# Kernel tuning notes

Measured on AMD Instinct MI355X. Metric: run time of the kernel, lower is better.

Reference implementation:

```python
import jax, jax.numpy as jnp
import numpy as np

B, IN_DIM, MEM = 8192, 4096, 256
MIN_TS, MAX_TS, EPS = 0.1, 10.0, 1e-6
LN_EPS = 1e-5


def setup_inputs() -> dict:
    key = jax.random.key(0)
    ks = jax.random.split(key, 10)
    std = 0.02
    d_in = MEM + IN_DIM  # 4352
    return {
        "x": jax.random.normal(ks[0], (B, IN_DIM), jnp.float32),
        "h": jax.random.normal(ks[1], (B, MEM), jnp.float32),
        # memory_target: Linear(d_in, 2*MEM) -> LN -> GELU -> Linear(2*MEM, MEM)
        "W1": std * jax.random.normal(ks[2], (d_in, 2 * MEM), jnp.float32),
        "b1": jnp.zeros((2 * MEM,), jnp.float32),
        "g1": jnp.ones((2 * MEM,), jnp.float32),
        "be1": jnp.zeros((2 * MEM,), jnp.float32),
        "W2": std * jax.random.normal(ks[3], (2 * MEM, MEM), jnp.float32),
        "b2": jnp.zeros((MEM,), jnp.float32),
        # decay_gate: Linear(d_in, MEM) -> sigmoid
        "Wd": std * jax.random.normal(ks[4], (d_in, MEM), jnp.float32),
        "bd": jnp.zeros((MEM,), jnp.float32),
        # input_gate: Linear(d_in, MEM) -> sigmoid
        "Wu": std * jax.random.normal(ks[5], (d_in, MEM), jnp.float32),
        "bu": jnp.zeros((MEM,), jnp.float32),
    }


def _layernorm(t, g, b):
    mu = jnp.mean(t, axis=-1, keepdims=True)
    var = jnp.mean(jnp.square(t - mu), axis=-1, keepdims=True)
    return (t - mu) * jax.lax.rsqrt(var + LN_EPS) * g + b


def reference(x, h, W1, b1, g1, be1, W2, b2, Wd, bd, Wu, bu):
    combined = jnp.concatenate([h, x], axis=-1)  # [B, MEM+IN_DIM]
    # memory_target branch: Linear -> LayerNorm -> GELU (exact) -> Linear -> tanh
    t = _layernorm(combined @ W1 + b1, g1, be1)
    t = jax.nn.gelu(t, approximate=False)
    h_candidate = jnp.tanh(t @ W2 + b2)  # [B, MEM]
    # gates
    decay = jax.nn.sigmoid(combined @ Wd + bd)
    update = jax.nn.sigmoid(combined @ Wu + bu)
    decay = MIN_TS + (MAX_TS - MIN_TS) * decay + EPS
    new_h = (1.0 - update) * (h / decay) + update * h_candidate
    # normalize_memory: rescale new_h to old h's L2 norm
    h_norm = jnp.maximum(jnp.linalg.norm(h, axis=-1, keepdims=True), EPS)
    nh_norm = jnp.maximum(jnp.linalg.norm(new_h, axis=-1, keepdims=True), 1e-12)
    new_h = new_h / nh_norm * h_norm
    return new_h
```

## Files before the change

kernel.cpp:

```cpp
#include <hip/hip_runtime.h>
#include <stdint.h>

typedef unsigned short u16;

#define B_ROWS 8192
#define IN_DIM 4096
#define MEM 256
#define D_IN 4352
#define N1 1024
#define K2 512
#define LN_EPS 1e-5f

typedef __attribute__((ext_vector_type(4))) float f32x4;
typedef __attribute__((ext_vector_type(4))) uint32_t u32x4;
typedef __attribute__((ext_vector_type(4))) unsigned short u16x4;
typedef __attribute__((ext_vector_type(8))) short bf16x8;

#define AS1(p) ((__attribute__((address_space(1))) void*)(p))
#define AS3(p) ((__attribute__((address_space(3))) void*)(p))

__device__ __forceinline__ float bf2f(u16 u) {
  union { uint32_t u; float f; } c; c.u = ((uint32_t)u) << 16; return c.f;
}
__device__ __forceinline__ u16 f2bf(float f) {
  union { float f; uint32_t u; } c; c.f = f;
  uint32_t r = (c.u + 0x7fffu + ((c.u >> 16) & 1u)) >> 16;
  return (u16)r;
}
__device__ __forceinline__ uint32_t fbits(float f) {
  union { float f; uint32_t u; } c; c.f = f; return c.u;
}
__device__ __forceinline__ uint32_t pack_rne(float a, float b) {
  return ((uint32_t)f2bf(b) << 16) | f2bf(a);
}
__device__ __forceinline__ uint32_t pack_trunc(float a, float b) {
  return (fbits(b) & 0xFFFF0000u) | (fbits(a) >> 16);
}

__global__ __launch_bounds__(256)
void prep_kernel(const float* __restrict__ W1, const float* __restrict__ Wd,
                 const float* __restrict__ Wu, const float* __restrict__ W2,
                 const float* __restrict__ h, const float* __restrict__ x,
                 u16* __restrict__ WT, u16* __restrict__ W2F, u16* __restrict__ Abf,
                 int pre) {
  __shared__ u16 tile[64][68];
  const int blk = blockIdx.x, t = threadIdx.x;
  if (blk < 1088) {
    int n0 = (blk & 15) * 64, k0 = (blk >> 4) * 64;
    const float* src; int srcN, ns0;
    if (n0 < 512)      { src = W1; srcN = 512; ns0 = n0; }
    else if (n0 < 768) { src = Wd; srcN = 256; ns0 = n0 - 512; }
    else               { src = Wu; srcN = 256; ns0 = n0 - 768; }
    int rr = t >> 4;
    int c4 = (t & 15) * 4;
#pragma unroll
    for (int i = 0; i < 4; i++) {
      int k = i * 16 + rr;
      f32x4 v = *(const f32x4*)&src[(size_t)(k0 + k) * srcN + ns0 + c4];
      tile[c4 + 0][k] = f2bf(v[0]);
      tile[c4 + 1][k] = f2bf(v[1]);
      tile[c4 + 2][k] = f2bf(v[2]);
      tile[c4 + 3][k] = f2bf(v[3]);
    }
    __syncthreads();
#pragma unroll
    for (int i = 0; i < 4; i++) {
      int n = i * 16 + rr;
      u16x4 w;
      w.x = tile[n][c4 + 0];
      w.y = tile[n][c4 + 1];
      w.z = tile[n][c4 + 2];
      w.w = tile[n][c4 + 3];
      if (pre) {
        int n16 = (n0 >> 4) + i;
        int kg = k0 + c4;
        int kstep = kg >> 5;
        int qq = (kg >> 3) & 3;
        int j0 = kg & 7;
        *(u16x4*)&WT[((size_t)(kstep * 64 + n16) * 64 + qq * 16 + rr) * 8 + j0] = w;
      } else {
        *(u16x4*)&WT[(size_t)(n0 + n) * D_IN + k0 + c4] = w;
      }
    }
  } else if (blk < 1104) {
    int kw = blk - 1088;
#pragma unroll
    for (int q = 0; q < 4; q++) {
      float v[8];
#pragma unroll
      for (int j = 0; j < 8; j++)
        v[j] = W2[(size_t)(kw * 32 + q * 8 + j) * 256 + t];
      u32x4 w;
      w.x = pack_rne(v[0], v[1]);
      w.y = pack_rne(v[2], v[3]);
      w.z = pack_rne(v[4], v[5]);
      w.w = pack_rne(v[6], v[7]);
      *(u32x4*)&W2F[(size_t)((kw * 4 + q) * 256 + t) * 8] = w;
    }
  } else {
    int b = blk - 1104;
    const float* src; int r, dcol;
    if (b < 1024) {
      int g = (b * 256 + t) * 8;
      src = h + g; r = g >> 8; dcol = g & 255;
    } else {
      int g = ((b - 1024) * 256 + t) * 8;
      src = x + g; r = g >> 12; dcol = MEM + (g & 4095);
    }
    f32x4 v0 = *(const f32x4*)src;
    f32x4 v1 = *(const f32x4*)(src + 4);
    u32x4 w;
    w.x = pack_rne(v0[0], v0[1]);
    w.y = pack_rne(v0[2], v0[3]);
    w.z = pack_rne(v1[0], v1[1]);
    w.w = pack_rne(v1[2], v1[3]);
    *(u32x4*)&Abf[(size_t)r * D_IN + dcol] = w;
  }
}

#define BAR() { asm volatile("" ::: "memory"); __builtin_amdgcn_s_barrier(); asm volatile("" ::: "memory"); }
#define VMW4() asm volatile("s_waitcnt vmcnt(4)" ::: "memory");

__global__ __launch_bounds__(512, 2)
void gemm1_pre256_kernel(const u16* __restrict__ Abf, const u16* __restrict__ WTF,
                         u16* __restrict__ G0, u16* __restrict__ G1, int klen) {
  __shared__ __attribute__((aligned(16))) u16 As[2][16384];
  const int t = threadIdx.x;
  const int lane = t & 63, wave = t >> 6;
  const int bid = (int)blockIdx.x;
  const int xcd = bid & 7;
  const int idx = bid >> 3;
  const int part = xcd >> 2;
  const int by = (xcd & 3) * 8 + (idx & 7);
  const int bx = idx >> 3;
  const int kbase = part * klen;
  u16* __restrict__ Gout = part ? G1 : G0;
  const int row0 = by * 256, col0 = bx * 256;
  const int q = lane >> 4, mrow = lane & 15;
  const int wm = wave >> 2, wn = wave & 3;
  const int NT = klen >> 6;

  int sr0, sc0_, sr1, sc1_;
  {
    int idx0 = t;        sr0 = idx0 >> 2; sc0_ = (idx0 & 3) ^ ((sr0 >> 1) & 3);
    int idx1 = 512 + t;  sr1 = idx1 >> 2; sc1_ = (idx1 & 3) ^ ((sr1 >> 1) & 3);
  }
  const u16* pa0 = Abf + (size_t)(row0 + sr0) * D_IN + sc0_ * 8;
  const u16* pa1 = Abf + (size_t)(row0 + sr1) * D_IN + sc1_ * 8;
  const int fsw = (mrow >> 1) & 3;

#define STAGE_A(buf, kk, kt)                                                            \
  __builtin_amdgcn_global_load_lds(AS1(pa0 + (kt) + (kk) * 32),                         \
      AS3(&As[buf][(kk) * 8192 + t * 8]), 16, 0, 0);                                    \
  __builtin_amdgcn_global_load_lds(AS1(pa1 + (kt) + (kk) * 32),                         \
      AS3(&As[buf][(kk) * 8192 + (512 + t) * 8]), 16, 0, 0);

  const u16* bptr = WTF + (size_t)(kbase >> 5) * 32768 + (bx * 16 + wn * 4) * 512 + lane * 8;

  f32x4 acc[8][4] = {};
  bf16x8 b0[4], b1[4];

  STAGE_A(0, 0, kbase)
  STAGE_A(0, 1, kbase)
#pragma unroll
  for (int nt = 0; nt < 4; nt++) b0[nt] = *(const bf16x8*)(bptr + nt * 512);
  VMW4();
  BAR();

  for (int tt = 0; tt < NT; ++tt) {
    const int cur = tt & 1, nxt = cur ^ 1;
    const int kn = kbase + (tt + 1) * 64;
    const bool pf = (tt + 1 < NT);

#pragma unroll
    for (int nt = 0; nt < 4; nt++) b1[nt] = *(const bf16x8*)(bptr + 32768 + nt * 512);
    if (pf) { STAGE_A(nxt, 0, kn) }

#define READ_A(kk, mh, areg)                                                            \
  _Pragma("unroll") for (int i = 0; i < 4; i++) {                                       \
    int arow = wm * 128 + ((mh) * 4 + i) * 16 + mrow;                                   \
    areg[i] = *(const bf16x8*)&As[cur][(kk) * 8192 + arow * 32 + (q ^ fsw) * 8];        \
  }
#define MFMA16(mh, breg)                                                                \
  __builtin_amdgcn_s_setprio(1);                                                        \
  _Pragma("unroll") for (int i = 0; i < 4; i++)                                         \
    _Pragma("unroll") for (int nt = 0; nt < 4; nt++)                                    \
      acc[(mh) * 4 + i][nt] =                                                           \
          __builtin_amdgcn_mfma_f32_16x16x32_bf16(a[i], breg[nt], acc[(mh) * 4 + i][nt], 0, 0, 0); \
  __builtin_amdgcn_s_setprio(0);

    {
      bf16x8 a[4];
      READ_A(0, 0, a)
      MFMA16(0, b0)
      READ_A(0, 1, a)
      MFMA16(1, b0)
    }
    if (pf) {
      STAGE_A(nxt, 1, kn)
#pragma unroll
      for (int nt = 0; nt < 4; nt++) b0[nt] = *(const bf16x8*)(bptr + 65536 + nt * 512);
    }
    {
      bf16x8 a[4];
      READ_A(1, 0, a)
      MFMA16(0, b1)
      READ_A(1, 1, a)
      MFMA16(1, b1)
    }
    if (pf) {
      VMW4();
      BAR();
    }
    bptr += 65536;
#undef READ_A
#undef MFMA16
  }

#pragma unroll
  for (int mt = 0; mt < 8; mt++) {
#pragma unroll
    for (int nt = 0; nt < 4; nt++) {
#pragma unroll
      for (int i = 0; i < 4; i++) {
        int row = row0 + wm * 128 + mt * 16 + q * 4 + i;
        int col = col0 + wn * 64 + nt * 16 + mrow;
        Gout[(size_t)row * N1 + col] = f2bf(acc[mt][nt][i]);
      }
    }
  }
}
#undef STAGE_A

__global__ __launch_bounds__(256, 4)
void gemm1_inline_kernel(const float* __restrict__ x, const float* __restrict__ h,
                         const u16* __restrict__ WT, u16* __restrict__ G0,
                         u16* __restrict__ G1, int klen) {
  __shared__ __attribute__((aligned(16))) u16 As[128 * 64];
  __shared__ __attribute__((aligned(16))) u16 Bs[128 * 64];
  const int t = threadIdx.x;
  const int lane = t & 63, wave = t >> 6;
  const int by = blockIdx.x & 63;
  const int bx = (blockIdx.x >> 6) & 7;
  const int part = blockIdx.x >> 9;
  const int kbase = part * klen;
  u16* __restrict__ Gout = part ? G1 : G0;
  const int row0 = by * 128, col0 = bx * 128;
  const int q = lane >> 4, mrow = lane & 15;
  const int wm = wave >> 1, wn = wave & 1;

  int ar[4], ac[4];
#pragma unroll
  for (int j = 0; j < 4; j++) {
    int idx = j * 256 + t;
    int r = idx >> 3;
    ar[j] = r;
    ac[j] = (idx & 7) ^ (r & 7);
  }
  f32x4 acc[4][4] = {};
  for (int k0 = kbase; k0 < kbase + klen; k0 += 64) {
#pragma unroll
    for (int j = 0; j < 4; j++) {
      const u16* gp = WT + (size_t)(col0 + ar[j]) * D_IN + k0 + ac[j] * 8;
      __builtin_amdgcn_global_load_lds(AS1(gp), AS3(&Bs[(j * 256 + t) * 8]), 16, 0, 0);
    }
#pragma unroll
    for (int j = 0; j < 4; j++) {
      int k = k0 + ac[j] * 8;
      const float* gp = (k < MEM) ? (h + (size_t)(row0 + ar[j]) * MEM + k)
                                  : (x + (size_t)(row0 + ar[j]) * IN_DIM + (k - MEM));
      f32x4 v0 = *(const f32x4*)gp;
      f32x4 v1 = *(const f32x4*)(gp + 4);
      u32x4 w;
      w.x = pack_trunc(v0[0], v0[1]);
      w.y = pack_trunc(v0[2], v0[3]);
      w.z = pack_trunc(v1[0], v1[1]);
      w.w = pack_trunc(v1[2], v1[3]);
      *(u32x4*)&As[(j * 256 + t) * 8] = w;
    }
    __syncthreads();
#pragma unroll
    for (int kk = 0; kk < 2; kk++) {
      bf16x8 a[4], b[4];
#pragma unroll
      for (int mt = 0; mt < 4; mt++) {
        int row = wm * 64 + mt * 16 + mrow;
        int p = (kk * 4 + q) ^ (mrow & 7);
        a[mt] = *(const bf16x8*)&As[row * 64 + p * 8];
      }
#pragma unroll
      for (int nt = 0; nt < 4; nt++) {
        int row = wn * 64 + nt * 16 + mrow;
        int p = (kk * 4 + q) ^ (mrow & 7);
        b[nt] = *(const bf16x8*)&Bs[row * 64 + p * 8];
      }
#pragma unroll
      for (int mt = 0; mt < 4; mt++) {
#pragma unroll
        for (int nt = 0; nt < 4; nt++) {
          acc[mt][nt] = __builtin_amdgcn_mfma_f32_16x16x32_bf16(a[mt], b[nt], acc[mt][nt], 0, 0, 0);
        }
      }
    }
    __syncthreads();
  }
#pragma unroll
  for (int mt = 0; mt < 4; mt++) {
#pragma unroll
    for (int nt = 0; nt < 4; nt++) {
#pragma unroll
      for (int i = 0; i < 4; i++) {
        int row = row0 + wm * 64 + mt * 16 + q * 4 + i;
        int col = col0 + wn * 64 + nt * 16 + mrow;
        Gout[(size_t)row * N1 + col] = f2bf(acc[mt][nt][i]);
      }
    }
  }
}

__global__ __launch_bounds__(256, 4)
void fused_ln_gemm2_kernel(const u16* __restrict__ G0, const u16* __restrict__ G1,
                           const u16* __restrict__ W2F, const float* __restrict__ h,
                           const float* __restrict__ b1v, const float* __restrict__ g1v,
                           const float* __restrict__ be1v, const float* __restrict__ b2,
                           const float* __restrict__ bd, const float* __restrict__ bu,
                           float* __restrict__ out, int nparts) {
  __shared__ __attribute__((aligned(16))) u16 As[16 * 512];
  __shared__ float redA[16][4], redB[16][4], scl[16];
  const int t = threadIdx.x, lane = t & 63, wave = t >> 6;
  const int q = lane >> 4, mrow = lane & 15;
  const int r0 = blockIdx.x * 16;

  {
    const int lr = t & 15;
    const int lc = t >> 4;
    float z[32];
    const u16* g0p = G0 + (size_t)(r0 + lr) * N1 + lc * 32;
    const u16* g1p = G1 + (size_t)(r0 + lr) * N1 + lc * 32;
    float s = 0.f, ss = 0.f;
#pragma unroll
    for (int j = 0; j < 4; j++) {
      u32x4 w0 = *(const u32x4*)(g0p + j * 8);
      u32x4 w1;
      if (nparts == 2) w1 = *(const u32x4*)(g1p + j * 8);
#pragma unroll
      for (int e = 0; e < 4; e++) {
        float lo = bf2f((u16)(w0[e] & 0xffff));
        float hi = bf2f((u16)(w0[e] >> 16));
        if (nparts == 2) {
          lo += bf2f((u16)(w1[e] & 0xffff));
          hi += bf2f((u16)(w1[e] >> 16));
        }
        int cb = lc * 32 + j * 8 + e * 2;
        lo += b1v[cb];
        hi += b1v[cb + 1];
        z[j * 8 + e * 2] = lo;
        z[j * 8 + e * 2 + 1] = hi;
        s += lo + hi;
        ss += lo * lo + hi * hi;
      }
    }
    s += __shfl_xor(s, 16, 64);  s += __shfl_xor(s, 32, 64);
    ss += __shfl_xor(ss, 16, 64); ss += __shfl_xor(ss, 32, 64);
    if (lane < 16) { redA[lr][wave] = s; redB[lr][wave] = ss; }
    __syncthreads();
    float S  = redA[lr][0] + redA[lr][1] + redA[lr][2] + redA[lr][3];
    float SS = redB[lr][0] + redB[lr][1] + redB[lr][2] + redB[lr][3];
    float mu = S * (1.0f / 512.0f);
    float var = SS * (1.0f / 512.0f) - mu * mu;
    float rstd = rsqrtf(var + LN_EPS);
#pragma unroll
    for (int j = 0; j < 4; j++) {
      u32x4 wpk;
#pragma unroll
      for (int e = 0; e < 4; e++) {
        int cb = lc * 32 + j * 8 + e * 2;
        float y0 = (z[j * 8 + e * 2] - mu) * rstd * g1v[cb] + be1v[cb];
        float y1 = (z[j * 8 + e * 2 + 1] - mu) * rstd * g1v[cb + 1] + be1v[cb + 1];
        float o0 = 0.5f * y0 * (1.0f + erff(y0 * 0.7071067811865475f));
        float o1 = 0.5f * y1 * (1.0f + erff(y1 * 0.7071067811865475f));
        wpk[e] = pack_rne(o0, o1);
      }
      int p = lc * 4 + j;
      int ps = p ^ (lr & 7);
      *(u32x4*)&As[lr * 512 + ps * 8] = wpk;
    }
  }
  __syncthreads();

  f32x4 acc[4] = {};
#pragma unroll
  for (int kw = 0; kw < 16; kw++) {
    int pa = (kw * 4 + q) ^ (mrow & 7);
    bf16x8 a = *(const bf16x8*)&As[mrow * 512 + pa * 8];
#pragma unroll
    for (int nt = 0; nt < 4; nt++) {
      const u16* bp = W2F + (size_t)((kw * 4 + q) * 256 + wave * 64 + nt * 16 + mrow) * 8;
      bf16x8 b = *(const bf16x8*)bp;
      acc[nt] = __builtin_amdgcn_mfma_f32_16x16x32_bf16(a, b, acc[nt], 0, 0, 0);
    }
  }
  __syncthreads();

  float snh[4], shh[4];
#pragma unroll
  for (int i = 0; i < 4; i++) {
    int r = q * 4 + i;
    size_t grow = (size_t)(r0 + r);
    float a_nh = 0.f, a_h = 0.f;
#pragma unroll
    for (int nt = 0; nt < 4; nt++) {
      int c = wave * 64 + nt * 16 + mrow;
      float hc = tanhf(acc[nt][i] + b2[c]);
      float zd = bf2f(G0[grow * N1 + 512 + c]);
      float zu = bf2f(G0[grow * N1 + 768 + c]);
      if (nparts == 2) {
        zd += bf2f(G1[grow * N1 + 512 + c]);
        zu += bf2f(G1[grow * N1 + 768 + c]);
      }
      zd += bd[c];
      zu += bu[c];
      float dec = 0.1f + 9.9f / (1.0f + expf(-zd)) + 1e-6f;
      float u = 1.0f / (1.0f + expf(-zu));
      float hv = h[grow * MEM + c];
      float nh = (1.0f - u) * (hv / dec) + u * hc;
      acc[nt][i] = nh;
      a_nh += nh * nh;
      a_h += hv * hv;
    }
    snh[i] = a_nh;
    shh[i] = a_h;
  }
#pragma unroll
  for (int m = 1; m <= 8; m <<= 1) {
#pragma unroll
    for (int i = 0; i < 4; i++) {
      snh[i] += __shfl_xor(snh[i], m, 64);
      shh[i] += __shfl_xor(shh[i], m, 64);
    }
  }
  if (mrow == 0) {
#pragma unroll
    for (int i = 0; i < 4; i++) {
      int r = q * 4 + i;
      redA[r][wave] = snh[i];
      redB[r][wave] = shh[i];
    }
  }
  __syncthreads();
  if (t < 16) {
    float tn = redA[t][0] + redA[t][1] + redA[t][2] + redA[t][3];
    float th = redB[t][0] + redB[t][1] + redB[t][2] + redB[t][3];
    float hn = fmaxf(sqrtf(th), 1e-6f);
    float nn = fmaxf(sqrtf(tn), 1e-12f);
    scl[t] = hn / nn;
  }
  __syncthreads();
#pragma unroll
  for (int i = 0; i < 4; i++) {
    int r = q * 4 + i;
    size_t grow = (size_t)(r0 + r);
    float sc = scl[r];
#pragma unroll
    for (int nt = 0; nt < 4; nt++) {
      int c = wave * 64 + nt * 16 + mrow;
      out[grow * MEM + c] = acc[nt][i] * sc;
    }
  }
}

extern "C" void kernel_launch(void* const* d_in, const int* in_sizes, int n_in,
                              void* d_out, int out_size, void* d_ws, size_t ws_size,
                              hipStream_t stream) {
  const float* x   = (const float*)d_in[0];
  const float* h   = (const float*)d_in[1];
  const float* W1  = (const float*)d_in[2];
  const float* b1  = (const float*)d_in[3];
  const float* g1  = (const float*)d_in[4];
  const float* be1 = (const float*)d_in[5];
  const float* W2  = (const float*)d_in[6];
  const float* b2  = (const float*)d_in[7];
  const float* Wd  = (const float*)d_in[8];
  const float* bd  = (const float*)d_in[9];
  const float* Wu  = (const float*)d_in[10];
  const float* bu  = (const float*)d_in[11];
  float* out = (float*)d_out;

  char* ws = (char*)d_ws;
  u16* WT  = (u16*)(ws);
  u16* W2F = (u16*)(ws + 8912896);
  u16* G0  = (u16*)(ws + 9175040);
  u16* G1  = (u16*)(ws + 25952256);
  u16* Abf = (u16*)(ws + 42729472);

  const int nparts = (ws_size >= 42729472u) ? 2 : 1;
  const int klen = D_IN / nparts;
  const bool use_pre = (ws_size >= 114032640u) && (nparts == 2);

  if (use_pre) {
    prep_kernel<<<18512, 256, 0, stream>>>(W1, Wd, Wu, W2, h, x, WT, W2F, Abf, 1);
    gemm1_pre256_kernel<<<256, 512, 0, stream>>>(Abf, WT, G0, G1, klen);
  } else {
    prep_kernel<<<1104, 256, 0, stream>>>(W1, Wd, Wu, W2, h, x, WT, W2F, Abf, 0);
    gemm1_inline_kernel<<<512 * nparts, 256, 0, stream>>>(x, h, WT, G0, G1, klen);
  }

  fused_ln_gemm2_kernel<<<B_ROWS / 16, 256, 0, stream>>>(G0, G1, W2F, h, b1, g1, be1,
                                                         b2, bd, bu, out, nparts);
}
```

Before: 346.5 us.

## Pre-tile bf16 activations into MFMA fragment layout and load A directly to registers

The prep kernel now writes the bf16 activation matrix in a K-chunked layout of 32-wide fragments, so each lane's MFMA A-operand is one contiguous 16-byte load. The GEMM1 kernel drops the LDS staging of A (global_load_lds, swizzle, barriers) and double-buffers both A and B fragments directly in registers across 32-wide K steps. This removes LDS traffic and synchronisation but raises register pressure, since 16 A fragments plus 8 B fragments are live per thread. Each wave also reloads A rows from global/L2 with no sharing through LDS, which may add global memory traffic.

```diff
diff --git a/kernel.cpp b/kernel.cpp
--- a/kernel.cpp
+++ b/kernel.cpp
@@ -99,13 +99,13 @@
     }
   } else {
     int b = blk - 1104;
-    const float* src; int r, dcol;
+    const float* src; int r, k0;
     if (b < 1024) {
       int g = (b * 256 + t) * 8;
-      src = h + g; r = g >> 8; dcol = g & 255;
+      src = h + g; r = g >> 8; k0 = g & 255;
     } else {
       int g = ((b - 1024) * 256 + t) * 8;
-      src = x + g; r = g >> 12; dcol = MEM + (g & 4095);
+      src = x + g; r = g >> 12; k0 = MEM + (g & 4095);
     }
     f32x4 v0 = *(const f32x4*)src;
     f32x4 v1 = *(const f32x4*)(src + 4);
@@ -114,17 +114,14 @@
     w.y = pack_rne(v0[2], v0[3]);
     w.z = pack_rne(v1[0], v1[1]);
     w.w = pack_rne(v1[2], v1[3]);
-    *(u32x4*)&Abf[(size_t)r * D_IN + dcol] = w;
-  }
-}
-
-#define BAR() { asm volatile("" ::: "memory"); __builtin_amdgcn_s_barrier(); asm volatile("" ::: "memory"); }
-#define VMW4() asm volatile("s_waitcnt vmcnt(4)" ::: "memory");
+    size_t off = ((size_t)(k0 >> 5) * 8192 + r) * 32 + (size_t)((k0 >> 3) & 3) * 8;
+    *(u32x4*)&Abf[off] = w;
+  }
+}
 
 __global__ __launch_bounds__(512, 2)
-void gemm1_pre256_kernel(const u16* __restrict__ Abf, const u16* __restrict__ WTF,
-                         u16* __restrict__ G0, u16* __restrict__ G1, int klen) {
-  __shared__ __attribute__((aligned(16))) u16 As[2][16384];
+void gemm1_reg_kernel(const u16* __restrict__ AF, const u16* __restrict__ WTF,
+                      u16* __restrict__ G0, u16* __restrict__ G1, int klen) {
   const int t = threadIdx.x;
   const int lane = t & 63, wave = t >> 6;
   const int bid = (int)blockIdx.x;
@@ -133,89 +130,56 @@
   const int part = xcd >> 2;
   const int by = (xcd & 3) * 8 + (idx & 7);
   const int bx = idx >> 3;
-  const int kbase = part * klen;
   u16* __restrict__ Gout = part ? G1 : G0;
   const int row0 = by * 256, col0 = bx * 256;
   const int q = lane >> 4, mrow = lane & 15;
   const int wm = wave >> 2, wn = wave & 3;
-  const int NT = klen >> 6;
-
-  int sr0, sc0_, sr1, sc1_;
-  {
-    int idx0 = t;        sr0 = idx0 >> 2; sc0_ = (idx0 & 3) ^ ((sr0 >> 1) & 3);
-    int idx1 = 512 + t;  sr1 = idx1 >> 2; sc1_ = (idx1 & 3) ^ ((sr1 >> 1) & 3);
-  }
-  const u16* pa0 = Abf + (size_t)(row0 + sr0) * D_IN + sc0_ * 8;
-  const u16* pa1 = Abf + (size_t)(row0 + sr1) * D_IN + sc1_ * 8;
-  const int fsw = (mrow >> 1) & 3;
-
-#define STAGE_A(buf, kk, kt)                                                            \
-  __builtin_amdgcn_global_load_lds(AS1(pa0 + (kt) + (kk) * 32),                         \
-      AS3(&As[buf][(kk) * 8192 + t * 8]), 16, 0, 0);                                    \
-  __builtin_amdgcn_global_load_lds(AS1(pa1 + (kt) + (kk) * 32),                         \
-      AS3(&As[buf][(kk) * 8192 + (512 + t) * 8]), 16, 0, 0);
-
-  const u16* bptr = WTF + (size_t)(kbase >> 5) * 32768 + (bx * 16 + wn * 4) * 512 + lane * 8;
+  const int NH = klen >> 5;
+  const int ks0 = part * NH;
+
+  const u16* abase = AF + ((size_t)(row0 + wm * 128 + mrow) * 4 + q) * 8 +
+                     (size_t)ks0 * 262144;
+  const u16* bbase = WTF + (size_t)(bx * 16 + wn * 4) * 512 + lane * 8 +
+                     (size_t)ks0 * 32768;
 
   f32x4 acc[8][4] = {};
-  bf16x8 b0[4], b1[4];
-
-  STAGE_A(0, 0, kbase)
-  STAGE_A(0, 1, kbase)
-#pragma unroll
-  for (int nt = 0; nt < 4; nt++) b0[nt] = *(const bf16x8*)(bptr + nt * 512);
-  VMW4();
-  BAR();
-
-  for (int tt = 0; tt < NT; ++tt) {
-    const int cur = tt & 1, nxt = cur ^ 1;
-    const int kn = kbase + (tt + 1) * 64;
-    const bool pf = (tt + 1 < NT);
-
-#pragma unroll
-    for (int nt = 0; nt < 4; nt++) b1[nt] = *(const bf16x8*)(bptr + 32768 + nt * 512);
-    if (pf) { STAGE_A(nxt, 0, kn) }
-
-#define READ_A(kk, mh, areg)                                                            \
-  _Pragma("unroll") for (int i = 0; i < 4; i++) {                                       \
-    int arow = wm * 128 + ((mh) * 4 + i) * 16 + mrow;                                   \
-    areg[i] = *(const bf16x8*)&As[cur][(kk) * 8192 + arow * 32 + (q ^ fsw) * 8];        \
-  }
-#define MFMA16(mh, breg)                                                                \
-  __builtin_amdgcn_s_setprio(1);                                                        \
-  _Pragma("unroll") for (int i = 0; i < 4; i++)                                         \
-    _Pragma("unroll") for (int nt = 0; nt < 4; nt++)                                    \
-      acc[(mh) * 4 + i][nt] =                                                           \
-          __builtin_amdgcn_mfma_f32_16x16x32_bf16(a[i], breg[nt], acc[(mh) * 4 + i][nt], 0, 0, 0); \
+  bf16x8 aA[8], aB[8], bA[4], bB[4];
+
+#define LOADA(bank, hh) {                                                     \
+    size_t ko = (size_t)(hh) * 262144;                                        \
+    _Pragma("unroll") for (int mt = 0; mt < 8; mt++)                          \
+      bank[mt] = *(const bf16x8*)(abase + ko + mt * 512);                     \
+  }
+#define LOADB(bank, hh) {                                                     \
+    size_t ko = (size_t)(hh) * 32768;                                         \
+    _Pragma("unroll") for (int nt = 0; nt < 4; nt++)                          \
+      bank[nt] = *(const bf16x8*)(bbase + ko + nt * 512);                     \
+  }
+#define MFMA32(abank, bbank)                                                  \
+  __builtin_amdgcn_s_setprio(1);                                              \
+  _Pragma("unroll") for (int mt = 0; mt < 8; mt++)                            \
+    _Pragma("unroll") for (int nt = 0; nt < 4; nt++)                          \
+      acc[mt][nt] = __builtin_amdgcn_mfma_f32_16x16x32_bf16(                  \
+          abank[mt], bbank[nt], acc[mt][nt], 0, 0, 0);                        \
   __builtin_amdgcn_s_setprio(0);
 
-    {
-      bf16x8 a[4];
-      READ_A(0, 0, a)
-      MFMA16(0, b0)
-      READ_A(0, 1, a)
-      MFMA16(1, b0)
-    }
-    if (pf) {
-      STAGE_A(nxt, 1, kn)
-#pragma unroll
-      for (int nt = 0; nt < 4; nt++) b0[nt] = *(const bf16x8*)(bptr + 65536 + nt * 512);
-    }
-    {
-      bf16x8 a[4];
-      READ_A(1, 0, a)
-      MFMA16(0, b1)
-      READ_A(1, 1, a)
-      MFMA16(1, b1)
-    }
-    if (pf) {
-      VMW4();
-      BAR();
-    }
-    bptr += 65536;
-#undef READ_A
-#undef MFMA16
-  }
+  LOADA(aA, 0)
+  LOADB(bA, 0)
+
+  for (int hh = 0; hh < NH; hh += 2) {
+    int h1 = (hh + 1 < NH) ? hh + 1 : hh;
+    LOADA(aB, h1)
+    LOADB(bB, h1)
+    MFMA32(aA, bA)
+    int h2 = (hh + 2 < NH) ? hh + 2 : hh;
+    LOADA(aA, h2)
+    LOADB(bA, h2)
+    MFMA32(aB, bB)
+    __builtin_amdgcn_s_barrier();
+  }
+#undef LOADA
+#undef LOADB
+#undef MFMA32
 
 #pragma unroll
   for (int mt = 0; mt < 8; mt++) {
@@ -230,7 +194,6 @@
     }
   }
 }
-#undef STAGE_A
 
 __global__ __launch_bounds__(256, 4)
 void gemm1_inline_kernel(const float* __restrict__ x, const float* __restrict__ h,
@@ -491,17 +454,17 @@
   u16* W2F = (u16*)(ws + 8912896);
   u16* G0  = (u16*)(ws + 9175040);
   u16* G1  = (u16*)(ws + 25952256);
-  u16* Abf = (u16*)(ws + 42729472);
+  u16* AF  = (u16*)(ws + 42729472);
 
   const int nparts = (ws_size >= 42729472u) ? 2 : 1;
   const int klen = D_IN / nparts;
   const bool use_pre = (ws_size >= 114032640u) && (nparts == 2);
 
   if (use_pre) {
-    prep_kernel<<<18512, 256, 0, stream>>>(W1, Wd, Wu, W2, h, x, WT, W2F, Abf, 1);
-    gemm1_pre256_kernel<<<256, 512, 0, stream>>>(Abf, WT, G0, G1, klen);
+    prep_kernel<<<18512, 256, 0, stream>>>(W1, Wd, Wu, W2, h, x, WT, W2F, AF, 1);
+    gemm1_reg_kernel<<<256, 512, 0, stream>>>(AF, WT, G0, G1, klen);
   } else {
-    prep_kernel<<<1104, 256, 0, stream>>>(W1, Wd, Wu, W2, h, x, WT, W2F, Abf, 0);
+    prep_kernel<<<1104, 256, 0, stream>>>(W1, Wd, Wu, W2, h, x, WT, W2F, AF, 0);
     gemm1_inline_kernel<<<512 * nparts, 256, 0, stream>>>(x, h, WT, G0, G1, klen);
   }
 
```

Result: slower. 362.4 us (+4.6%).
